# Optimization experiments

Hardware: AMD Instinct MI355X
Metric: run time of the kernel (lower is better)

## Reference

```python
import jax, jax.numpy as jnp
import numpy as np

B, D_IN, D_OUT, Q_DIM = 8192, 400, 100, 10


def setup_inputs() -> dict:
    key = jax.random.key(0)
    kx, kw = jax.random.split(key)
    X = jax.random.normal(kx, (B, D_IN, Q_DIM), dtype=jnp.float32)
    # FRMap weight: randn(d_out, d_in) / sqrt(d_in)
    W = jax.random.normal(kw, (D_OUT, D_IN), dtype=jnp.float32) / (D_IN ** 0.5)
    return {"X": X, "W": W}


def reference(X, W):
    # FRMap: Y[b] = W @ X[b]  -> (B, d_out, q)
    Y = jnp.einsum('oi,biq->boq', W, X)
    # ReOrth: reduced QR of each tall-skinny (d_out, q) matrix, keep Q
    Q, _ = jnp.linalg.qr(Y, mode='reduced')  # (B, d_out, q)
    return Q
```

## Files before the change

kernel.cpp:

```cpp
#include <hip/hip_runtime.h>
#include <math.h>

#define BATCHES 8192
#define D_IN    400
#define D_OUT   100
#define QD      10
#define KT      64
#define NKT     7
#define MTILES  7
#define WFSZ    (NKT * MTILES * 2 * 64 * 8)
#define XB      648
#define NW      4
#define WCH     512
#define WHALF   (14 * WCH)

using bf16x8 = __attribute__((ext_vector_type(8))) short;
using f32x4  = __attribute__((ext_vector_type(4))) float;

template <int CTRL>
__device__ __forceinline__ float dpp_add(float x) {
  int s = __builtin_amdgcn_update_dpp(0, __builtin_bit_cast(int, x),
                                      CTRL, 0xF, 0xF, true);
  return x + __builtin_bit_cast(float, s);
}

__device__ __forceinline__ float wsum64(float x) {
  x = dpp_add<0x111>(x);
  x = dpp_add<0x112>(x);
  x = dpp_add<0x114>(x);
  x = dpp_add<0x118>(x);
  x = dpp_add<0x142>(x);
  x = dpp_add<0x143>(x);
  return __builtin_bit_cast(float,
      __builtin_amdgcn_readlane(__builtin_bit_cast(int, x), 63));
}

__device__ __forceinline__ float lane_bcast(float x, int lane) {
  return __builtin_bit_cast(float,
      __builtin_amdgcn_readlane(__builtin_bit_cast(int, x), lane));
}

__device__ __forceinline__ void lds_barrier() {
  asm volatile("s_waitcnt lgkmcnt(0)" ::: "memory");
  __builtin_amdgcn_s_barrier();
  __builtin_amdgcn_sched_barrier(0);
}

__global__ __launch_bounds__(256) void wprep_kernel(const float* __restrict__ W,
                                                    short* __restrict__ wfh,
                                                    short* __restrict__ wfl) {
  const int e = blockIdx.x * 256 + threadIdx.x;
  if (e >= WFSZ) return;
  const int j = e & 7, lane = (e >> 3) & 63, ks = (e >> 9) & 1, mtkt = e >> 10;
  const int kt = mtkt / MTILES, mt = mtkt - kt * MTILES;
  const int o = mt * 16 + (lane & 15);
  const int k = kt * KT + ks * 32 + (lane >> 4) * 8 + j;
  const float w = (o < D_OUT && k < D_IN) ? W[o * D_IN + k] : 0.f;
  __bf16 h = (__bf16)w;
  float hf = (float)h;
  __bf16 l = (__bf16)(w - hf);
  wfh[e] = __builtin_bit_cast(short, h);
  wfl[e] = __builtin_bit_cast(short, l);
}

__device__ __forceinline__ void qr_and_store(const f32x4* acc, float* stg,
                                             float* dst, int lane, int col,
                                             int quad) {
  if (col < QD) {
    #pragma unroll
    for (int mt = 0; mt < MTILES; ++mt)
      #pragma unroll
      for (int rr = 0; rr < 4; ++rr) {
        const int o = mt * 16 + quad * 4 + rr;
        if (o < D_OUT) stg[o * QD + col] = acc[mt][rr];
      }
  }
  const int r = lane;
  float a0[QD], a1[QD];
  #pragma unroll
  for (int q = 0; q < QD; ++q) a0[q] = stg[r * QD + q];
  const bool has1 = (r + 64) < D_OUT;
  #pragma unroll
  for (int q = 0; q < QD; ++q) a1[q] = has1 ? stg[(r + 64) * QD + q] : 0.f;

  float v0[QD], v1[QD], tau[QD];
  #pragma unroll
  for (int j = 0; j < QD; ++j) {
    float cj0  = (r >= j) ? a0[j] : 0.f;
    float part = cj0 * cj0 + a1[j] * a1[j];
    float sig  = wsum64(part);
    float alpha = lane_bcast(a0[j], j);
    float nrm  = __builtin_amdgcn_sqrtf(sig);
    float aab  = fabsf(alpha);
    float rn   = __builtin_amdgcn_rcpf(nrm);
    float rd   = __builtin_amdgcn_rcpf(aab + nrm);
    float sgn  = (alpha >= 0.f) ? 1.f : -1.f;
    float tj   = (sig > 0.f) ? (1.f + aab * rn) : 0.f;
    float inv  = (sig > 0.f) ? sgn * rd : 0.f;
    tau[j] = tj;
    v0[j]  = (r == j) ? 1.f : ((r > j) ? a0[j] * inv : 0.f);
    v1[j]  = a1[j] * inv;
    #pragma unroll
    for (int k = j + 1; k < QD; ++k) {
      float p = v0[j] * a0[k] + v1[j] * a1[k];
      float s = wsum64(p) * tj;
      a0[k] -= s * v0[j];
      a1[k] -= s * v1[j];
    }
  }
  float q0[QD], q1[QD];
  #pragma unroll
  for (int c = 0; c < QD; ++c) { q0[c] = (r == c) ? 1.f : 0.f; q1[c] = 0.f; }
  #pragma unroll
  for (int j = QD - 1; j >= 0; --j) {
    #pragma unroll
    for (int c = j; c < QD; ++c) {
      float p = v0[j] * q0[c] + v1[j] * q1[c];
      float s = wsum64(p) * tau[j];
      q0[c] -= s * v0[j];
      q1[c] -= s * v1[j];
    }
  }
  #pragma unroll
  for (int c = 0; c < QD; ++c) stg[r * QD + c] = q0[c];
  if (has1) {
    #pragma unroll
    for (int c = 0; c < QD; ++c) stg[(r + 64) * QD + c] = q1[c];
  }
  const float4* src = (const float4*)stg;
  float4* d4 = (float4*)dst;
  #pragma unroll
  for (int u = r; u < (D_OUT * QD) / 4; u += 64) d4[u] = src[u];
}

__global__ __launch_bounds__(256, 4) void fused_kernel(const float* __restrict__ X,
                                                       const short* __restrict__ wfh,
                                                       const short* __restrict__ wfl,
                                                       float* __restrict__ out) {
  __shared__ __align__(16) float xstg[NW * 2 * XB];
  __shared__ __align__(16) short wtile[WHALF];
  const int tid  = threadIdx.x;
  const int lane = tid & 63;
  const int wv   = __builtin_amdgcn_readfirstlane(tid >> 6);
  const long b0  = (long)blockIdx.x * (NW * 2) + wv * 2;
  float* xs = xstg + wv * (2 * XB);
  const int col = lane & 15, quad = lane >> 4;

  f32x4 acc0[MTILES], acc1[MTILES];
  #pragma unroll
  for (int t = 0; t < MTILES; ++t) {
    acc0[t] = (f32x4){0.f, 0.f, 0.f, 0.f};
    acc1[t] = (f32x4){0.f, 0.f, 0.f, 0.f};
  }

  bf16x8 wst[4];
  auto wload = [&](int kt, int ks) {
    #pragma unroll
    for (int i = 0; i < 4; ++i) {
      const int c = wv + 4 * i;
      if (c < 14) {
        const short* pl = (c < 7) ? wfh : wfl;
        const int m = (c < 7) ? c : c - 7;
        wst[i] = *(const bf16x8*)(pl + ((long)(kt * 7 + m) * 2 + ks) * WCH + lane * 8);
      }
    }
  };
  auto wcommit = [&]() {
    #pragma unroll
    for (int i = 0; i < 4; ++i) {
      const int c = wv + 4 * i;
      if (c < 14) *(bf16x8*)&wtile[c * WCH + lane * 8] = wst[i];
    }
  };

  float4 pre[5];
  auto xpre = [&](int kt) {
    const int nk0 = kt * KT;
    const int vf4 = (nk0 + KT <= D_IN) ? 160 : ((D_IN - nk0) * QD) / 4;
    #pragma unroll
    for (int u = 0; u < 5; ++u) {
      const int idx = lane + u * 64;
      const int bsel = idx >= 160 ? 1 : 0;
      const int within = idx - bsel * 160;
      float4 v = {0.f, 0.f, 0.f, 0.f};
      if (within < vf4)
        v = *(const float4*)(X + (b0 + bsel) * (long)(D_IN * QD) + nk0 * QD + within * 4);
      pre[u] = v;
    }
  };
  auto xcommit = [&]() {
    #pragma unroll
    for (int u = 0; u < 5; ++u) {
      const int idx = lane + u * 64;
      const int bsel = idx >= 160 ? 1 : 0;
      const int within = idx - bsel * 160;
      *(float4*)&xs[bsel * XB + within * 4] = pre[u];
    }
  };

  auto computeHalf = [&](int ks) {
    bf16x8 b0h, b0l, b1h, b1l;
    #pragma unroll
    for (int m = 0; m < 8; ++m) {
      const int fo = (ks * 32 + quad * 8 + m) * QD + col;
      float x0 = xs[fo];
      float x1 = xs[XB + fo];
      __bf16 h0 = (__bf16)x0; float f0 = (float)h0; __bf16 g0 = (__bf16)(x0 - f0);
      __bf16 h1 = (__bf16)x1; float f1 = (float)h1; __bf16 g1 = (__bf16)(x1 - f1);
      b0h[m] = __builtin_bit_cast(short, h0); b0l[m] = __builtin_bit_cast(short, g0);
      b1h[m] = __builtin_bit_cast(short, h1); b1l[m] = __builtin_bit_cast(short, g1);
    }
    #pragma unroll
    for (int mt = 0; mt < MTILES; ++mt) {
      bf16x8 ah = *(const bf16x8*)&wtile[mt * WCH + lane * 8];
      bf16x8 al = *(const bf16x8*)&wtile[(7 + mt) * WCH + lane * 8];
      acc0[mt] = __builtin_amdgcn_mfma_f32_16x16x32_bf16(ah, b0h, acc0[mt], 0, 0, 0);
      acc0[mt] = __builtin_amdgcn_mfma_f32_16x16x32_bf16(al, b0h, acc0[mt], 0, 0, 0);
      acc0[mt] = __builtin_amdgcn_mfma_f32_16x16x32_bf16(ah, b0l, acc0[mt], 0, 0, 0);
      acc1[mt] = __builtin_amdgcn_mfma_f32_16x16x32_bf16(ah, b1h, acc1[mt], 0, 0, 0);
      acc1[mt] = __builtin_amdgcn_mfma_f32_16x16x32_bf16(al, b1h, acc1[mt], 0, 0, 0);
      acc1[mt] = __builtin_amdgcn_mfma_f32_16x16x32_bf16(ah, b1l, acc1[mt], 0, 0, 0);
    }
  };

  wload(0, 0);
  xpre(0);
  wcommit();
  lds_barrier();

  #pragma unroll 1
  for (int kt = 0; kt < NKT; ++kt) {
    wload(kt, 1);
    xcommit();
    if (kt + 1 < NKT) xpre(kt + 1);
    computeHalf(0);
    lds_barrier();
    wcommit();
    lds_barrier();
    if (kt + 1 < NKT) wload(kt + 1, 0);
    computeHalf(1);
    lds_barrier();
    if (kt + 1 < NKT) wcommit();
    lds_barrier();
  }

  qr_and_store(acc0, xs, out + b0 * (long)(D_OUT * QD), lane, col, quad);
  qr_and_store(acc1, xs, out + (b0 + 1) * (long)(D_OUT * QD), lane, col, quad);
}

extern "C" void kernel_launch(void* const* d_in, const int* in_sizes, int n_in,
                              void* d_out, int out_size, void* d_ws, size_t ws_size,
                              hipStream_t stream) {
  const float* X = (const float*)d_in[0];
  const float* W = (const float*)d_in[1];
  float* out = (float*)d_out;
  short* wfh = (short*)d_ws;
  short* wfl = wfh + WFSZ;
  hipLaunchKernelGGL(wprep_kernel, dim3((WFSZ + 255) / 256), dim3(256), 0, stream,
                     W, wfh, wfl);
  hipLaunchKernelGGL(fused_kernel, dim3(BATCHES / (NW * 2)), dim3(256), 0, stream,
                     X, wfh, wfl, out);
}
```

Before: 273.7 us.

## Stream W tiles directly into double-buffered LDS via global_load_lds

Replaces the register-staged W loads (global load into VGPRs, then LDS store) with direct global-to-LDS async loads into a double-buffered W tile. While one half of the K tile is computed, the next half is loading. This cuts the loop from four barriers per K tile to two, and removes the VGPR staging and LDS write instructions. The doubled LDS footprint forces the occupancy hint down from 4 to 3 blocks per CU, so less latency hiding comes from extra waves.

```diff
diff --git a/kernel.cpp b/kernel.cpp
--- a/kernel.cpp
+++ b/kernel.cpp
@@ -40,10 +40,10 @@
       __builtin_amdgcn_readlane(__builtin_bit_cast(int, x), lane));
 }
 
-__device__ __forceinline__ void lds_barrier() {
-  asm volatile("s_waitcnt lgkmcnt(0)" ::: "memory");
-  __builtin_amdgcn_s_barrier();
-  __builtin_amdgcn_sched_barrier(0);
+__device__ __forceinline__ void gload_lds16(const short* g, short* l) {
+  __builtin_amdgcn_global_load_lds(
+      (const __attribute__((address_space(1))) void*)g,
+      (__attribute__((address_space(3))) void*)l, 16, 0, 0);
 }
 
 __global__ __launch_bounds__(256) void wprep_kernel(const float* __restrict__ W,
@@ -133,12 +133,12 @@
   for (int u = r; u < (D_OUT * QD) / 4; u += 64) d4[u] = src[u];
 }
 
-__global__ __launch_bounds__(256, 4) void fused_kernel(const float* __restrict__ X,
+__global__ __launch_bounds__(256, 3) void fused_kernel(const float* __restrict__ X,
                                                        const short* __restrict__ wfh,
                                                        const short* __restrict__ wfl,
                                                        float* __restrict__ out) {
   __shared__ __align__(16) float xstg[NW * 2 * XB];
-  __shared__ __align__(16) short wtile[WHALF];
+  __shared__ __align__(16) short wtile[2 * WHALF];
   const int tid  = threadIdx.x;
   const int lane = tid & 63;
   const int wv   = __builtin_amdgcn_readfirstlane(tid >> 6);
@@ -153,23 +153,16 @@
     acc1[t] = (f32x4){0.f, 0.f, 0.f, 0.f};
   }
 
-  bf16x8 wst[4];
-  auto wload = [&](int kt, int ks) {
+  auto wissue = [&](int kt, int ks, int half) {
     #pragma unroll
     for (int i = 0; i < 4; ++i) {
       const int c = wv + 4 * i;
       if (c < 14) {
         const short* pl = (c < 7) ? wfh : wfl;
         const int m = (c < 7) ? c : c - 7;
-        wst[i] = *(const bf16x8*)(pl + ((long)(kt * 7 + m) * 2 + ks) * WCH + lane * 8);
+        gload_lds16(pl + ((long)(kt * MTILES + m) * 2 + ks) * WCH + lane * 8,
+                    &wtile[half * WHALF + c * WCH]);
       }
-    }
-  };
-  auto wcommit = [&]() {
-    #pragma unroll
-    for (int i = 0; i < 4; ++i) {
-      const int c = wv + 4 * i;
-      if (c < 14) *(bf16x8*)&wtile[c * WCH + lane * 8] = wst[i];
     }
   };
 
@@ -198,7 +191,7 @@
     }
   };
 
-  auto computeHalf = [&](int ks) {
+  auto computeHalf = [&](int ks, int half) {
     bf16x8 b0h, b0l, b1h, b1l;
     #pragma unroll
     for (int m = 0; m < 8; ++m) {
@@ -210,10 +203,11 @@
       b0h[m] = __builtin_bit_cast(short, h0); b0l[m] = __builtin_bit_cast(short, g0);
       b1h[m] = __builtin_bit_cast(short, h1); b1l[m] = __builtin_bit_cast(short, g1);
     }
+    const short* wb = &wtile[half * WHALF];
     #pragma unroll
     for (int mt = 0; mt < MTILES; ++mt) {
-      bf16x8 ah = *(const bf16x8*)&wtile[mt * WCH + lane * 8];
-      bf16x8 al = *(const bf16x8*)&wtile[(7 + mt) * WCH + lane * 8];
+      bf16x8 ah = *(const bf16x8*)(wb + mt * WCH + lane * 8);
+      bf16x8 al = *(const bf16x8*)(wb + (7 + mt) * WCH + lane * 8);
       acc0[mt] = __builtin_amdgcn_mfma_f32_16x16x32_bf16(ah, b0h, acc0[mt], 0, 0, 0);
       acc0[mt] = __builtin_amdgcn_mfma_f32_16x16x32_bf16(al, b0h, acc0[mt], 0, 0, 0);
       acc0[mt] = __builtin_amdgcn_mfma_f32_16x16x32_bf16(ah, b0l, acc0[mt], 0, 0, 0);
@@ -223,25 +217,32 @@
     }
   };
 
-  wload(0, 0);
+  wissue(0, 0, 0);
+  __builtin_amdgcn_sched_barrier(0);
   xpre(0);
-  wcommit();
-  lds_barrier();
+  asm volatile("s_waitcnt vmcnt(5)" ::: "memory");
+  __builtin_amdgcn_s_barrier();
+  __builtin_amdgcn_sched_barrier(0);
 
   #pragma unroll 1
   for (int kt = 0; kt < NKT; ++kt) {
-    wload(kt, 1);
     xcommit();
-    if (kt + 1 < NKT) xpre(kt + 1);
-    computeHalf(0);
-    lds_barrier();
-    wcommit();
-    lds_barrier();
-    if (kt + 1 < NKT) wload(kt + 1, 0);
-    computeHalf(1);
-    lds_barrier();
-    if (kt + 1 < NKT) wcommit();
-    lds_barrier();
+    wissue(kt, 1, 1);
+    computeHalf(0, 0);
+    asm volatile("s_waitcnt vmcnt(0)" ::: "memory");
+    __builtin_amdgcn_s_barrier();
+    __builtin_amdgcn_sched_barrier(0);
+    if (kt + 1 < NKT) {
+      wissue(kt + 1, 0, 0);
+      __builtin_amdgcn_sched_barrier(0);
+      xpre(kt + 1);
+    }
+    computeHalf(1, 1);
+    if (kt + 1 < NKT) {
+      asm volatile("s_waitcnt vmcnt(5)" ::: "memory");
+      __builtin_amdgcn_s_barrier();
+      __builtin_amdgcn_sched_barrier(0);
+    }
   }
 
   qr_and_store(acc0, xs, out + b0 * (long)(D_OUT * QD), lane, col, quad);
```

After: 220.8 us. -19.3%, faster.
